# Optimization experiments

Measured on AMD Instinct MI355X. Metric: run time of the kernel, lower is better.

## Reference

```python
import jax, jax.numpy as jnp
import numpy as np

B, S, E, H, V, T = 64, 64, 256, 512, 50000, 32
SOS, PAD = 1, 0


def setup_inputs() -> dict:
    key = jax.random.key(0)
    ks = jax.random.split(key, 12)
    sc = 0.05
    embedding = jax.random.normal(ks[0], (V, E), jnp.float32) * sc
    embedding = embedding.at[PAD].set(0.0)  # padding_idx row is zero
    inp = {
        "encoder_hidden": jax.random.normal(ks[1], (1, B, H), jnp.float32),
        "target": jax.random.randint(ks[2], (B, T), 0, V),
        "target_length": jax.random.randint(ks[3], (B,), 1, T + 1),
        "encoder_outputs": jax.random.normal(ks[4], (B, S, H), jnp.float32),
        "embedding": embedding,
        "w_ih": jax.random.normal(ks[5], (3 * H, E), jnp.float32) * sc,
        "w_hh": jax.random.normal(ks[6], (3 * H, H), jnp.float32) * sc,
        "b_ih": jnp.zeros((3 * H,), jnp.float32),
        "b_hh": jnp.zeros((3 * H,), jnp.float32),
        "attn_w": jax.random.normal(ks[7], (H, H), jnp.float32) * sc,  # Attention 'general' W
        "Wa": jax.random.normal(ks[8], (H, 2 * H), jnp.float32) * sc,  # concat projection (no bias)
        "fc_w": jax.random.normal(ks[9], (V, H), jnp.float32) * sc,
        "fc_b": jnp.zeros((V,), jnp.float32),
    }
    return inp


def _gru_cell(x, h, w_ih, w_hh, b_ih, b_hh):
    # PyTorch GRU cell math. x: [B,E], h: [B,H]
    gi = x @ w_ih.T + b_ih          # [B,3H]
    gh = h @ w_hh.T + b_hh          # [B,3H]
    i_r, i_z, i_n = jnp.split(gi, 3, axis=-1)
    h_r, h_z, h_n = jnp.split(gh, 3, axis=-1)
    r = jax.nn.sigmoid(i_r + h_r)
    z = jax.nn.sigmoid(i_z + h_z)
    n = jnp.tanh(i_n + r * h_n)
    return (1.0 - z) * n + z * h


def reference(encoder_hidden, target, target_length, encoder_outputs, embedding,
              w_ih, w_hh, b_ih, b_hh, attn_w, Wa, fc_w, fc_b):
    h0 = encoder_hidden[0]                                   # [B,H]
    # Luong 'general' attention: precompute W_attn @ encoder_outputs once
    enc_proj = jnp.einsum("bsh,gh->bsg", encoder_outputs, attn_w)  # [B,S,H]
    init_input = jnp.full((B,), SOS, dtype=jnp.int32)

    def step(carry, _):
        dec_in, h = carry
        x = embedding[dec_in]                                # [B,E]
        h_new = _gru_cell(x, h, w_ih, w_hh, b_ih, b_hh)      # [B,H]
        scores = jnp.einsum("bh,bsh->bs", h_new, enc_proj)   # [B,S]
        attn_weights = jax.nn.softmax(scores, axis=-1)
        context = jnp.einsum("bs,bsh->bh", attn_weights, encoder_outputs)
        concat = jnp.concatenate([h_new, context], axis=-1)  # [B,2H]
        concat_out = jnp.tanh(concat @ Wa.T)                 # [B,H]
        logits = jax.nn.log_softmax(concat_out @ fc_w.T + fc_b, axis=-1)  # [B,V]
        nxt = jnp.argmax(logits, axis=-1).astype(jnp.int32)  # topk(1) -> greedy
        return (nxt, h_new), logits

    (_, h_fin), outs = jax.lax.scan(step, (init_input, h0), None, length=T)
    decoder_outputs = jnp.transpose(outs, (1, 0, 2))          # [B,T,V]
    return decoder_outputs, h_fin[None]                       # ([B,T,V], [1,B,H])
```

## Files before the change

kernel.cpp:

```cpp
#include <hip/hip_runtime.h>
#include <math.h>

#define B_ 64
#define S_ 64
#define E_ 256
#define H_ 512
#define V_ 50000
#define T_ 32
#define SOS_ 1


__global__ __launch_bounds__(256) void build_wbig(
    const float* __restrict__ w_ih, const float* __restrict__ w_hh,
    const float* __restrict__ b_ih, const float* __restrict__ b_hh,
    float* __restrict__ WbigT, float* __restrict__ biasBig)
{
    int g = blockIdx.x * 256 + threadIdx.x;
    if (g < 2048 * 768) {
        int n = g / 768, k = g % 768;
        int j = n >> 2, c = n & 3;
        float v = 0.f;
        if (c == 0)      v = (k < 256) ? w_ih[j * 256 + k]          : w_hh[j * 512 + (k - 256)];
        else if (c == 1) v = (k < 256) ? w_ih[(512 + j) * 256 + k]  : w_hh[(512 + j) * 512 + (k - 256)];
        else if (c == 2) v = (k < 256) ? w_ih[(1024 + j) * 256 + k] : 0.f;
        else             v = (k < 256) ? 0.f                        : w_hh[(1024 + j) * 512 + (k - 256)];
        WbigT[g] = v;
    }
    if (g < 2048) {
        int j = g >> 2, c = g & 3;
        float bv;
        if (c == 0)      bv = b_ih[j] + b_hh[j];
        else if (c == 1) bv = b_ih[512 + j] + b_hh[512 + j];
        else if (c == 2) bv = b_ih[1024 + j];
        else             bv = b_hh[1024 + j];
        biasBig[g] = bv;
    }
}

__global__ __launch_bounds__(256) void transpose_aw(
    const float* __restrict__ attn_w, float* __restrict__ awT)
{
    int idx = blockIdx.x * 256 + threadIdx.x;
    int h = idx >> 9, g = idx & 511;
    awT[idx] = attn_w[g * 512 + h];
}

__global__ __launch_bounds__(256) void init_state(
    const float* __restrict__ enc_hidden, float* __restrict__ hbuf0,
    int* __restrict__ dec_in)
{
    int idx = blockIdx.x * 256 + threadIdx.x;
    if (idx < B_ * H_) hbuf0[idx] = enc_hidden[idx];
    if (idx < B_) dec_in[idx] = SOS_;
}

template <int MODE>
__global__ __launch_bounds__(256) void gemm64(
    const float* __restrict__ A, const float* __restrict__ W,
    float* __restrict__ C, const float* __restrict__ bias,
    int N, int Kfull, int kchunk,
    const float* __restrict__ emb, const int* __restrict__ tok,
    const float* __restrict__ hcur, long long ldc)
{
    __shared__ float As[64][68];
    __shared__ float Ws[64][68];
    const int tid = threadIdx.x;
    const int n0 = blockIdx.x * 64;
    const int k0base = blockIdx.y * kchunk;
    const int tm = tid & 15;
    const int tn = tid >> 4;
    float acc[4][4] = {{0.f}};

    for (int kt = 0; kt < kchunk; kt += 64) {
        const int k0 = k0base + kt;
        #pragma unroll
        for (int r = 0; r < 4; ++r) {
            int idx = tid + r * 256;
            int m = idx >> 4;
            int kk = (idx & 15) << 2;
            float4 v;
            if (MODE == 0) {
                int k = k0 + kk;
                if (k < 256) v = *(const float4*)&emb[(size_t)tok[m] * 256 + k];
                else         v = *(const float4*)&hcur[m * 512 + (k - 256)];
            } else {
                v = *(const float4*)&A[(size_t)m * Kfull + k0 + kk];
            }
            As[kk + 0][m] = v.x; As[kk + 1][m] = v.y;
            As[kk + 2][m] = v.z; As[kk + 3][m] = v.w;
        }
        #pragma unroll
        for (int r = 0; r < 4; ++r) {
            int idx = tid + r * 256;
            int n = idx >> 4;
            int kk = (idx & 15) << 2;
            int row = n0 + n;
            float4 v = make_float4(0.f, 0.f, 0.f, 0.f);
            if (MODE != 2 || row < N)
                v = *(const float4*)&W[(size_t)row * Kfull + k0 + kk];
            Ws[kk + 0][n] = v.x; Ws[kk + 1][n] = v.y;
            Ws[kk + 2][n] = v.z; Ws[kk + 3][n] = v.w;
        }
        __syncthreads();
        #pragma unroll
        for (int kk = 0; kk < 64; ++kk) {
            float4 a = *(const float4*)&As[kk][tm << 2];
            float4 w = *(const float4*)&Ws[kk][tn << 2];
            acc[0][0] += a.x * w.x; acc[0][1] += a.x * w.y;
            acc[0][2] += a.x * w.z; acc[0][3] += a.x * w.w;
            acc[1][0] += a.y * w.x; acc[1][1] += a.y * w.y;
            acc[1][2] += a.y * w.z; acc[1][3] += a.y * w.w;
            acc[2][0] += a.z * w.x; acc[2][1] += a.z * w.y;
            acc[2][2] += a.z * w.z; acc[2][3] += a.z * w.w;
            acc[3][0] += a.w * w.x; acc[3][1] += a.w * w.y;
            acc[3][2] += a.w * w.z; acc[3][3] += a.w * w.w;
        }
        __syncthreads();
    }

    if (MODE == 2) {
        #pragma unroll
        for (int i = 0; i < 4; ++i) {
            int m = (tm << 2) + i;
            #pragma unroll
            for (int j2 = 0; j2 < 4; ++j2) {
                int v = n0 + (tn << 2) + j2;
                if (v < N) C[(long long)m * ldc + v] = acc[i][j2] + bias[v];
            }
        }
    } else {
        float* Cp = C + (size_t)blockIdx.y * 64 * N;
        #pragma unroll
        for (int i = 0; i < 4; ++i) {
            int m = (tm << 2) + i;
            #pragma unroll
            for (int j2 = 0; j2 < 4; ++j2) {
                Cp[(size_t)m * N + n0 + (tn << 2) + j2] = acc[i][j2];
            }
        }
    }
}

__global__ __launch_bounds__(512) void combine_kernel(
    const float* __restrict__ gP, const float* __restrict__ bb,
    const float* __restrict__ hcur, float* __restrict__ hnxt,
    float* __restrict__ concatA)
{
    int idx = blockIdx.x * 512 + threadIdx.x;
    int b = idx >> 9, j = idx & 511;
    int base = b * 2048 + (j << 2);
    const int SP = 64 * 2048;
    float g0 = gP[base + 0] + gP[SP + base + 0] + gP[2 * SP + base + 0] + bb[(j << 2) + 0];
    float g1 = gP[base + 1] + gP[SP + base + 1] + gP[2 * SP + base + 1] + bb[(j << 2) + 1];
    float g2 = gP[base + 2] + gP[SP + base + 2] + gP[2 * SP + base + 2] + bb[(j << 2) + 2];
    float g3 = gP[base + 3] + gP[SP + base + 3] + gP[2 * SP + base + 3] + bb[(j << 2) + 3];
    float r = 1.f / (1.f + expf(-g0));
    float z = 1.f / (1.f + expf(-g1));
    float n = tanhf(g2 + r * g3);
    float hv = hcur[idx];
    float h2 = (1.f - z) * n + z * hv;
    hnxt[idx] = h2;
    concatA[b * 1024 + j] = h2;
}

__global__ __launch_bounds__(512) void attn_kernel(
    const float* __restrict__ qP, const float* __restrict__ enc,
    float* __restrict__ concatA)
{
    int b = blockIdx.x;
    int tid = threadIdx.x;
    __shared__ float q[512];
    __shared__ float aw[64];
    q[tid] = qP[b * 512 + tid] + qP[64 * 512 + b * 512 + tid];
    __syncthreads();

    int wv = tid >> 6, ln = tid & 63;
    #pragma unroll
    for (int si = 0; si < 8; ++si) {
        int s = (wv << 3) + si;
        const float* er = enc + ((size_t)(b * 64 + s)) * 512;
        float p = 0.f;
        #pragma unroll
        for (int i = 0; i < 8; ++i) p += q[ln + (i << 6)] * er[ln + (i << 6)];
        for (int off = 32; off; off >>= 1) p += __shfl_down(p, off);
        if (ln == 0) aw[s] = p;
    }
    __syncthreads();
    if (tid < 64) {
        float v = aw[tid], m = v;
        for (int off = 32; off; off >>= 1) m = fmaxf(m, __shfl_xor(m, off));
        float e = expf(v - m);
        float ssum = e;
        for (int off = 32; off; off >>= 1) ssum += __shfl_xor(ssum, off);
        aw[tid] = e / ssum;
    }
    __syncthreads();
    float c = 0.f;
    const float* eb = enc + (size_t)b * 64 * 512 + tid;
    for (int s = 0; s < 64; ++s) c += aw[s] * eb[s * 512];
    concatA[b * 1024 + 512 + tid] = c;
}

__global__ __launch_bounds__(512) void tanh_combine(
    const float* __restrict__ cgP, float* __restrict__ Abuf)
{
    int idx = blockIdx.x * 512 + threadIdx.x;
    const int SP = 64 * 512;
    float v = cgP[idx] + cgP[SP + idx] + cgP[2 * SP + idx] + cgP[3 * SP + idx];
    Abuf[idx] = tanhf(v);
}

__global__ __launch_bounds__(1024) void lsm_kernel(
    float* __restrict__ out, int t, int* __restrict__ dec_in)
{
    int b = blockIdx.x;
    int tid = threadIdx.x;
    float* row = out + (size_t)b * T_ * V_ + (size_t)t * V_;
    __shared__ float sv[1024];
    __shared__ int si_[1024];

    float lm = -INFINITY;
    int li = 0;
    for (int v = tid; v < V_; v += 1024) {
        float x = row[v];
        if (x > lm) { lm = x; li = v; }
    }
    sv[tid] = lm; si_[tid] = li;
    __syncthreads();
    for (int s = 512; s; s >>= 1) {
        if (tid < s) {
            float o = sv[tid + s]; int oi = si_[tid + s];
            if (o > sv[tid] || (o == sv[tid] && oi < si_[tid])) { sv[tid] = o; si_[tid] = oi; }
        }
        __syncthreads();
    }
    float M = sv[0];
    int amax = si_[0];
    __syncthreads();

    float ls = 0.f;
    for (int v = tid; v < V_; v += 1024) ls += expf(row[v] - M);
    sv[tid] = ls;
    __syncthreads();
    for (int s = 512; s; s >>= 1) {
        if (tid < s) sv[tid] += sv[tid + s];
        __syncthreads();
    }
    float logZ = M + logf(sv[0]);

    for (int v = tid; v < V_; v += 1024) row[v] -= logZ;
    if (tid == 0) dec_in[b] = amax;
}

__global__ __launch_bounds__(256) void final_copy(
    const float* __restrict__ hfin, float* __restrict__ dst)
{
    int idx = blockIdx.x * 256 + threadIdx.x;
    if (idx < B_ * H_) dst[idx] = hfin[idx];
}

extern "C" void kernel_launch(void* const* d_in, const int* in_sizes, int n_in,
                              void* d_out, int out_size, void* d_ws, size_t ws_size,
                              hipStream_t stream)
{
    const float* enc_hidden = (const float*)d_in[0];
    const float* enc    = (const float*)d_in[3];
    const float* emb    = (const float*)d_in[4];
    const float* w_ih   = (const float*)d_in[5];
    const float* w_hh   = (const float*)d_in[6];
    const float* b_ih   = (const float*)d_in[7];
    const float* b_hh   = (const float*)d_in[8];
    const float* attn_w = (const float*)d_in[9];
    const float* Wa     = (const float*)d_in[10];
    const float* fc_w   = (const float*)d_in[11];
    const float* fc_b   = (const float*)d_in[12];
    float* out = (float*)d_out;
    float* ws  = (float*)d_ws;

    float* WbigT   = ws;
    float* biasBig = WbigT + 1572864;
    float* awT     = biasBig + 2048;
    float* hbuf0   = awT + 262144;
    float* hbuf1   = hbuf0 + 32768;
    float* gatesP  = hbuf1 + 32768;
    float* qP      = gatesP + 393216;
    float* concatA = qP + 65536;
    float* cgP     = concatA + 65536;
    float* Abuf    = cgP + 131072;
    int*   dec_in  = (int*)(Abuf + 32768);

    build_wbig<<<6144, 256, 0, stream>>>(w_ih, w_hh, b_ih, b_hh, WbigT, biasBig);
    transpose_aw<<<1024, 256, 0, stream>>>(attn_w, awT);
    init_state<<<128, 256, 0, stream>>>(enc_hidden, hbuf0, dec_in);

    for (int t = 0; t < T_; ++t) {
        float* hcur = (t & 1) ? hbuf1 : hbuf0;
        float* hnxt = (t & 1) ? hbuf0 : hbuf1;

        gemm64<0><<<dim3(32, 3), 256, 0, stream>>>(
            nullptr, WbigT, gatesP, nullptr, 2048, 768, 256,
            emb, dec_in, hcur, 0);

        combine_kernel<<<64, 512, 0, stream>>>(gatesP, biasBig, hcur, hnxt, concatA);

        gemm64<1><<<dim3(8, 2), 256, 0, stream>>>(
            hnxt, awT, qP, nullptr, 512, 512, 256,
            nullptr, nullptr, nullptr, 0);

        attn_kernel<<<64, 512, 0, stream>>>(qP, enc, concatA);

        gemm64<1><<<dim3(8, 4), 256, 0, stream>>>(
            concatA, Wa, cgP, nullptr, 512, 1024, 256,
            nullptr, nullptr, nullptr, 0);

        tanh_combine<<<64, 512, 0, stream>>>(cgP, Abuf);

        gemm64<2><<<dim3(782, 1), 256, 0, stream>>>(
            Abuf, fc_w, out + (size_t)t * V_, fc_b, V_, 512, 512,
            nullptr, nullptr, nullptr, (long long)T_ * V_);

        lsm_kernel<<<64, 1024, 0, stream>>>(out, t, dec_in);
    }

    final_copy<<<128, 256, 0, stream>>>(hbuf0, out + (size_t)B_ * T_ * V_);
}
```

Baseline: 5.720 ms.

## Use bf16 MFMA for vocab projection with fused softmax stats and fp32 argmax refine

Converts fc_w to bf16 once and computes the 50000-wide logits with MFMA 16x16x32 bf16 instructions. The kernel also emits per-chunk max, argmax and sum-exp partials, so the separate log-softmax pass becomes a small reduction plus a normalize pass. Greedy argmax is recomputed in fp32 for chunks within a margin of the maximum, which keeps the token choice close to exact. The smaller GEMMs are also split into more K-chunks to raise parallelism. The trade-off is bf16 rounding in the logits, a heuristic argmax margin, and extra workspace use.

```diff
diff --git a/kernel.cpp b/kernel.cpp
--- a/kernel.cpp
+++ b/kernel.cpp
@@ -8,7 +8,19 @@
 #define V_ 50000
 #define T_ 32
 #define SOS_ 1
-
+#define NCHUNK 196
+static const long long LDCV = (long long)T_ * V_;
+
+typedef unsigned short u16;
+typedef u16   u16x8  __attribute__((ext_vector_type(8)));
+typedef short bf16x8 __attribute__((ext_vector_type(8)));
+typedef float f32x4  __attribute__((ext_vector_type(4)));
+
+static __device__ __forceinline__ u16 f2bf(float f) {
+    unsigned u = __float_as_uint(f);
+    unsigned r = (u + 0x7FFFu + ((u >> 16) & 1u)) >> 16;
+    return (u16)r;
+}
 
 __global__ __launch_bounds__(256) void build_wbig(
     const float* __restrict__ w_ih, const float* __restrict__ w_hh,
@@ -52,6 +64,18 @@
     int idx = blockIdx.x * 256 + threadIdx.x;
     if (idx < B_ * H_) hbuf0[idx] = enc_hidden[idx];
     if (idx < B_) dec_in[idx] = SOS_;
+}
+
+__global__ __launch_bounds__(256) void conv_fcw(
+    const float* __restrict__ fc_w, u16* __restrict__ fcwb)
+{
+    size_t i = (size_t)(blockIdx.x * 256 + threadIdx.x) * 8;
+    float4 a = *(const float4*)&fc_w[i];
+    float4 b = *(const float4*)&fc_w[i + 4];
+    u16x8 o;
+    o[0] = f2bf(a.x); o[1] = f2bf(a.y); o[2] = f2bf(a.z); o[3] = f2bf(a.w);
+    o[4] = f2bf(b.x); o[5] = f2bf(b.y); o[6] = f2bf(b.z); o[7] = f2bf(b.w);
+    *(u16x8*)&fcwb[i] = o;
 }
 
 template <int MODE>
@@ -150,10 +174,15 @@
     int b = idx >> 9, j = idx & 511;
     int base = b * 2048 + (j << 2);
     const int SP = 64 * 2048;
-    float g0 = gP[base + 0] + gP[SP + base + 0] + gP[2 * SP + base + 0] + bb[(j << 2) + 0];
-    float g1 = gP[base + 1] + gP[SP + base + 1] + gP[2 * SP + base + 1] + bb[(j << 2) + 1];
-    float g2 = gP[base + 2] + gP[SP + base + 2] + gP[2 * SP + base + 2] + bb[(j << 2) + 2];
-    float g3 = gP[base + 3] + gP[SP + base + 3] + gP[2 * SP + base + 3] + bb[(j << 2) + 3];
+    float g0 = bb[(j << 2) + 0], g1 = bb[(j << 2) + 1];
+    float g2 = bb[(j << 2) + 2], g3 = bb[(j << 2) + 3];
+    #pragma unroll
+    for (int p = 0; p < 6; ++p) {
+        g0 += gP[p * SP + base + 0];
+        g1 += gP[p * SP + base + 1];
+        g2 += gP[p * SP + base + 2];
+        g3 += gP[p * SP + base + 3];
+    }
     float r = 1.f / (1.f + expf(-g0));
     float z = 1.f / (1.f + expf(-g1));
     float n = tanhf(g2 + r * g3);
@@ -171,7 +200,9 @@
     int tid = threadIdx.x;
     __shared__ float q[512];
     __shared__ float aw[64];
-    q[tid] = qP[b * 512 + tid] + qP[64 * 512 + b * 512 + tid];
+    const int SP = 64 * 512;
+    q[tid] = qP[b * 512 + tid] + qP[SP + b * 512 + tid]
+           + qP[2 * SP + b * 512 + tid] + qP[3 * SP + b * 512 + tid];
     __syncthreads();
 
     int wv = tid >> 6, ln = tid & 63;
@@ -202,12 +233,219 @@
 }
 
 __global__ __launch_bounds__(512) void tanh_combine(
-    const float* __restrict__ cgP, float* __restrict__ Abuf)
+    const float* __restrict__ cgP, float* __restrict__ Abuf,
+    u16* __restrict__ Abufb)
 {
     int idx = blockIdx.x * 512 + threadIdx.x;
     const int SP = 64 * 512;
-    float v = cgP[idx] + cgP[SP + idx] + cgP[2 * SP + idx] + cgP[3 * SP + idx];
-    Abuf[idx] = tanhf(v);
+    float v = 0.f;
+    #pragma unroll
+    for (int p = 0; p < 8; ++p) v += cgP[p * SP + idx];
+    float th = tanhf(v);
+    Abuf[idx] = th;
+    Abufb[idx] = f2bf(th);
+}
+
+__global__ __launch_bounds__(256) void logits_mfma(
+    const u16* __restrict__ Abufb, const u16* __restrict__ fcwb,
+    const float* __restrict__ fc_b, float* __restrict__ outp,
+    float* __restrict__ pmax, int* __restrict__ pidx, float* __restrict__ psum)
+{
+    __shared__ u16 sA[64 * 512];
+    const int tid = threadIdx.x;
+    const int wv = tid >> 6, lane = tid & 63;
+    const int nb = blockIdx.x * 256;
+    const int col16 = lane & 15, grp = lane >> 4;
+
+    #pragma unroll
+    for (int i = 0; i < 16; ++i) {
+        int c = tid + i * 256;
+        int m = c >> 6;
+        int cb = (c & 63) << 4;
+        int sb = cb ^ ((m & 7) << 4);
+        *(u16x8*)((char*)sA + m * 1024 + sb) =
+            *(const u16x8*)(Abufb + m * 512 + (cb >> 1));
+    }
+    __syncthreads();
+
+    int nfb[4]; bool val[4];
+    #pragma unroll
+    for (int fn = 0; fn < 4; ++fn) {
+        nfb[fn] = nb + wv * 64 + fn * 16;
+        val[fn] = nfb[fn] < V_;
+    }
+    const u16* wptr[4];
+    #pragma unroll
+    for (int fn = 0; fn < 4; ++fn) {
+        size_t rowi = val[fn] ? (size_t)(nfb[fn] + col16) : 0;
+        wptr[fn] = fcwb + rowi * 512 + (grp << 3);
+    }
+
+    f32x4 acc[4][4];
+    #pragma unroll
+    for (int a = 0; a < 4; ++a)
+        #pragma unroll
+        for (int b2 = 0; b2 < 4; ++b2) acc[a][b2] = (f32x4){0.f, 0.f, 0.f, 0.f};
+
+    bf16x8 bcur[4];
+    #pragma unroll
+    for (int fn = 0; fn < 4; ++fn) bcur[fn] = *(const bf16x8*)(wptr[fn]);
+
+    for (int kt = 0; kt < 16; ++kt) {
+        bf16x8 bnxt[4];
+        int ktn = (kt + 1 < 16) ? kt + 1 : 15;
+        #pragma unroll
+        for (int fn = 0; fn < 4; ++fn)
+            bnxt[fn] = *(const bf16x8*)(wptr[fn] + ktn * 32);
+        bf16x8 af[4];
+        int kb = kt * 64 + (grp << 4);
+        #pragma unroll
+        for (int fm = 0; fm < 4; ++fm) {
+            int mg = fm * 16 + col16;
+            af[fm] = *(const bf16x8*)((const char*)sA + mg * 1024 + (kb ^ ((mg & 7) << 4)));
+        }
+        #pragma unroll
+        for (int fm = 0; fm < 4; ++fm)
+            #pragma unroll
+            for (int fn = 0; fn < 4; ++fn)
+                acc[fm][fn] = __builtin_amdgcn_mfma_f32_16x16x32_bf16(
+                    af[fm], bcur[fn], acc[fm][fn], 0, 0, 0);
+        #pragma unroll
+        for (int fn = 0; fn < 4; ++fn) bcur[fn] = bnxt[fn];
+    }
+    __syncthreads();
+
+    float* wmaxp = (float*)sA;
+    int*   widxp = (int*)(sA + 512);
+    float* wsump = (float*)(sA + 1024);
+
+    float bias[4];
+    #pragma unroll
+    for (int fn = 0; fn < 4; ++fn) bias[fn] = val[fn] ? fc_b[nfb[fn] + col16] : 0.f;
+
+    #pragma unroll
+    for (int fm = 0; fm < 4; ++fm) {
+        #pragma unroll
+        for (int r = 0; r < 4; ++r) {
+            int mrow = fm * 16 + grp * 4 + r;
+            float best = -INFINITY; int bi = 0;
+            float vv[4];
+            #pragma unroll
+            for (int fn = 0; fn < 4; ++fn) {
+                float v = -INFINITY;
+                if (val[fn]) {
+                    v = acc[fm][fn][r] + bias[fn];
+                    int n = nfb[fn] + col16;
+                    outp[(size_t)mrow * LDCV + n] = v;
+                    if (v > best || (v == best && n < bi)) { best = v; bi = n; }
+                }
+                vv[fn] = v;
+            }
+            #pragma unroll
+            for (int d = 1; d < 16; d <<= 1) {
+                float ov = __shfl_xor(best, d); int oi = __shfl_xor(bi, d);
+                if (ov > best || (ov == best && oi < bi)) { best = ov; bi = oi; }
+            }
+            float s = 0.f;
+            #pragma unroll
+            for (int fn = 0; fn < 4; ++fn)
+                if (val[fn]) s += __expf(vv[fn] - best);
+            #pragma unroll
+            for (int d = 1; d < 16; d <<= 1) s += __shfl_xor(s, d);
+            if (col16 == 0) {
+                wmaxp[wv * 64 + mrow] = best;
+                widxp[wv * 64 + mrow] = bi;
+                wsump[wv * 64 + mrow] = s;
+            }
+        }
+    }
+    __syncthreads();
+    if (tid < 64) {
+        float gm = -INFINITY; int gi = 0;
+        #pragma unroll
+        for (int w = 0; w < 4; ++w) {
+            float v = wmaxp[w * 64 + tid]; int ii = widxp[w * 64 + tid];
+            if (v > gm || (v == gm && ii < gi)) { gm = v; gi = ii; }
+        }
+        float gs = 0.f;
+        #pragma unroll
+        for (int w = 0; w < 4; ++w)
+            gs += wsump[w * 64 + tid] * __expf(wmaxp[w * 64 + tid] - gm);
+        pmax[tid * NCHUNK + blockIdx.x] = gm;
+        pidx[tid * NCHUNK + blockIdx.x] = gi;
+        psum[tid * NCHUNK + blockIdx.x] = gs;
+    }
+}
+
+__global__ __launch_bounds__(256) void szrefine(
+    const float* __restrict__ pmax, const int* __restrict__ pidx,
+    const float* __restrict__ psum, const float* __restrict__ Abuf,
+    const float* __restrict__ fc_w, const float* __restrict__ fc_b,
+    float* __restrict__ logZ_arr, int* __restrict__ dec_in)
+{
+    int b = blockIdx.x, tid = threadIdx.x;
+    __shared__ float sv[256];
+    __shared__ int   si2[256];
+    __shared__ float A[512];
+    __shared__ int clist[96];
+    __shared__ int ccnt;
+
+    float pm = (tid < NCHUNK) ? pmax[b * NCHUNK + tid] : -INFINITY;
+    sv[tid] = pm; __syncthreads();
+    for (int st = 128; st; st >>= 1) { if (tid < st) sv[tid] = fmaxf(sv[tid], sv[tid + st]); __syncthreads(); }
+    float Mb = sv[0]; __syncthreads();
+
+    float sc = (tid < NCHUNK) ? psum[b * NCHUNK + tid] * __expf(pm - Mb) : 0.f;
+    sv[tid] = sc; __syncthreads();
+    for (int st = 128; st; st >>= 1) { if (tid < st) sv[tid] += sv[tid + st]; __syncthreads(); }
+    if (tid == 0) { logZ_arr[b] = Mb + logf(sv[0]); ccnt = 0; }
+    __syncthreads();
+
+    if (tid < NCHUNK && pm >= Mb - 0.05f) {
+        int s2 = atomicAdd(&ccnt, 1);
+        if (s2 < 96) clist[s2] = tid;
+    }
+    A[tid] = Abuf[b * 512 + tid];
+    A[tid + 256] = Abuf[b * 512 + 256 + tid];
+    __syncthreads();
+
+    int nc = min(ccnt, 96);
+    float best = -INFINITY; int bidx = 0x7fffffff;
+    for (int ci = 0; ci < nc; ++ci) {
+        int n = clist[ci] * 256 + tid;
+        if (n < V_) {
+            const float* wr = fc_w + (size_t)n * 512;
+            float d = fc_b[n];
+            #pragma unroll 8
+            for (int k = 0; k < 512; k += 4) {
+                float4 w4 = *(const float4*)&wr[k];
+                d += A[k] * w4.x + A[k + 1] * w4.y + A[k + 2] * w4.z + A[k + 3] * w4.w;
+            }
+            if (d > best || (d == best && n < bidx)) { best = d; bidx = n; }
+        }
+    }
+    sv[tid] = best; si2[tid] = bidx; __syncthreads();
+    for (int st = 128; st; st >>= 1) {
+        if (tid < st) {
+            float o = sv[tid + st]; int oi = si2[tid + st];
+            if (o > sv[tid] || (o == sv[tid] && oi < si2[tid])) { sv[tid] = o; si2[tid] = oi; }
+        }
+        __syncthreads();
+    }
+    if (tid == 0) dec_in[b] = si2[0];
+}
+
+__global__ __launch_bounds__(256) void norm_kernel(
+    float* __restrict__ outp , const float* __restrict__ logZ_arr)
+{
+    int idx = blockIdx.x * 256 + threadIdx.x;
+    int b = idx / 12500;
+    int j = idx - b * 12500;
+    float z = logZ_arr[b];
+    float4* p = (float4*)(outp + (size_t)b * LDCV) + j;
+    float4 v = *p;
+    v.x -= z; v.y -= z; v.z -= z; v.w -= z;
+    *p = v;
 }
 
 __global__ __launch_bounds__(1024) void lsm_kernel(
@@ -277,49 +515,66 @@
     float* out = (float*)d_out;
     float* ws  = (float*)d_ws;
 
-    float* WbigT   = ws;
-    float* biasBig = WbigT + 1572864;
-    float* awT     = biasBig + 2048;
-    float* hbuf0   = awT + 262144;
-    float* hbuf1   = hbuf0 + 32768;
-    float* gatesP  = hbuf1 + 32768;
-    float* qP      = gatesP + 393216;
-    float* concatA = qP + 65536;
-    float* cgP     = concatA + 65536;
-    float* Abuf    = cgP + 131072;
-    int*   dec_in  = (int*)(Abuf + 32768);
+    size_t off = 0;
+    float* WbigT   = ws + off; off += 1572864;
+    float* biasBig = ws + off; off += 2048;
+    float* awT     = ws + off; off += 262144;
+    float* hbuf0   = ws + off; off += 32768;
+    float* hbuf1   = ws + off; off += 32768;
+    float* gatesP  = ws + off; off += 6 * 64 * 2048;
+    float* qP      = ws + off; off += 4 * 64 * 512;
+    float* concatA = ws + off; off += 65536;
+    float* cgP     = ws + off; off += 8 * 64 * 512;
+    float* Abuf    = ws + off; off += 32768;
+    u16*   Abufb   = (u16*)(ws + off); off += 16384;
+    float* pmax    = ws + off; off += 64 * NCHUNK;
+    int*   pidx    = (int*)(ws + off); off += 64 * NCHUNK;
+    float* psum    = ws + off; off += 64 * NCHUNK;
+    float* logZ_a  = ws + off; off += 64;
+    int*   dec_in  = (int*)(ws + off); off += 64;
+    u16*   fcwb    = (u16*)(ws + off);
+    size_t need_bytes = (off + 12800000) * 4;
+    const bool big = ws_size >= need_bytes;
 
     build_wbig<<<6144, 256, 0, stream>>>(w_ih, w_hh, b_ih, b_hh, WbigT, biasBig);
     transpose_aw<<<1024, 256, 0, stream>>>(attn_w, awT);
     init_state<<<128, 256, 0, stream>>>(enc_hidden, hbuf0, dec_in);
+    if (big) conv_fcw<<<12500, 256, 0, stream>>>(fc_w, fcwb);
 
     for (int t = 0; t < T_; ++t) {
         float* hcur = (t & 1) ? hbuf1 : hbuf0;
         float* hnxt = (t & 1) ? hbuf0 : hbuf1;
 
-        gemm64<0><<<dim3(32, 3), 256, 0, stream>>>(
-            nullptr, WbigT, gatesP, nullptr, 2048, 768, 256,
+        gemm64<0><<<dim3(32, 6), 256, 0, stream>>>(
+            nullptr, WbigT, gatesP, nullptr, 2048, 768, 128,
             emb, dec_in, hcur, 0);
 
         combine_kernel<<<64, 512, 0, stream>>>(gatesP, biasBig, hcur, hnxt, concatA);
 
-        gemm64<1><<<dim3(8, 2), 256, 0, stream>>>(
-            hnxt, awT, qP, nullptr, 512, 512, 256,
+        gemm64<1><<<dim3(8, 4), 256, 0, stream>>>(
+            hnxt, awT, qP, nullptr, 512, 512, 128,
             nullptr, nullptr, nullptr, 0);
 
         attn_kernel<<<64, 512, 0, stream>>>(qP, enc, concatA);
 
-        gemm64<1><<<dim3(8, 4), 256, 0, stream>>>(
-            concatA, Wa, cgP, nullptr, 512, 1024, 256,
+        gemm64<1><<<dim3(8, 8), 256, 0, stream>>>(
+            concatA, Wa, cgP, nullptr, 512, 1024, 128,
             nullptr, nullptr, nullptr, 0);
 
-        tanh_combine<<<64, 512, 0, stream>>>(cgP, Abuf);
-
-        gemm64<2><<<dim3(782, 1), 256, 0, stream>>>(
-            Abuf, fc_w, out + (size_t)t * V_, fc_b, V_, 512, 512,
-            nullptr, nullptr, nullptr, (long long)T_ * V_);
-
-        lsm_kernel<<<64, 1024, 0, stream>>>(out, t, dec_in);
+        tanh_combine<<<64, 512, 0, stream>>>(cgP, Abuf, Abufb);
+
+        if (big) {
+            logits_mfma<<<NCHUNK, 256, 0, stream>>>(
+                Abufb, fcwb, fc_b, out + (size_t)t * V_, pmax, pidx, psum);
+            szrefine<<<64, 256, 0, stream>>>(
+                pmax, pidx, psum, Abuf, fc_w, fc_b, logZ_a, dec_in);
+            norm_kernel<<<3125, 256, 0, stream>>>(out + (size_t)t * V_, logZ_a);
+        } else {
+            gemm64<2><<<dim3(782, 1), 256, 0, stream>>>(
+                Abuf, fc_w, out + (size_t)t * V_, fc_b, V_, 512, 512,
+                nullptr, nullptr, nullptr, LDCV);
+            lsm_kernel<<<64, 1024, 0, stream>>>(out, t, dec_in);
+        }
     }
 
     final_copy<<<128, 256, 0, stream>>>(hbuf0, out + (size_t)B_ * T_ * V_);
```

After: 7.182 ms. 25.6% more time.
